# Optimization experiments

Measured on AMD Instinct MI355X. Metric: run time of the kernel, lower is better.

The kernel has to match this reference:

```python
import jax, jax.numpy as jnp
from jax import lax
import numpy as np

B = 512
IN_CAPS, OUT_CAPS, IN_DIM, OUT_DIM, ITERS = 32 * 6 * 6, 10, 8, 16, 3
EPS = 1e-8


def setup_inputs() -> dict:
    key = jax.random.key(0)
    ks = jax.random.split(key, 12)
    inp = {
        "x": jax.random.normal(ks[0], (B, 1, 28, 28), dtype=jnp.float32),
        "conv1_w": jax.random.normal(ks[1], (256, 1, 9, 9), dtype=jnp.float32) * 0.05,
        "conv1_b": jnp.zeros((256,), dtype=jnp.float32),
        "conv2_w": jax.random.normal(ks[2], (256, 256, 9, 9), dtype=jnp.float32) * 0.02,
        "conv2_b": jnp.zeros((256,), dtype=jnp.float32),
        "W": jax.random.normal(ks[3], (IN_CAPS, OUT_CAPS, IN_DIM, OUT_DIM), dtype=jnp.float32) * 0.1,
        "d1_w": jax.random.normal(ks[4], (OUT_DIM * OUT_CAPS, 512), dtype=jnp.float32) * 0.05,
        "d1_b": jnp.zeros((512,), dtype=jnp.float32),
        "d2_w": jax.random.normal(ks[5], (512, 1024), dtype=jnp.float32) * 0.05,
        "d2_b": jnp.zeros((1024,), dtype=jnp.float32),
        "d3_w": jax.random.normal(ks[6], (1024, 28 * 28), dtype=jnp.float32) * 0.05,
        "d3_b": jnp.zeros((28 * 28,), dtype=jnp.float32),
    }
    return inp


def _squash(s):
    # s2/(1+s2) * s/sqrt(s2+eps), norm over last dim
    s2 = jnp.sum(s * s, axis=-1, keepdims=True)
    return s2 / (1.0 + s2) * (s / jnp.sqrt(s2 + EPS))


def _conv(x, w, b, stride):
    y = lax.conv_general_dilated(x, w, (stride, stride), "VALID",
                                 dimension_numbers=("NCHW", "OIHW", "NCHW"))
    return y + b[None, :, None, None]


def reference(x, conv1_w, conv1_b, conv2_w, conv2_b, W,
              d1_w, d1_b, d2_w, d2_b, d3_w, d3_b):
    h = jax.nn.relu(_conv(x, conv1_w, conv1_b, 1))          # [B,256,20,20]
    h = _conv(h, conv2_w, conv2_b, 2)                       # [B,256,6,6]
    u = h.reshape(h.shape[0], 8, IN_CAPS).transpose(0, 2, 1)  # [B,1152,8]
    u = _squash(u)

    # dynamic routing
    u_hat = jnp.einsum("ijnm,bin->bijm", W, u)              # [B,1152,10,16]
    b_log = jnp.zeros((u.shape[0], IN_CAPS, OUT_CAPS), dtype=u.dtype)
    v = None
    for _ in range(ITERS):
        c = jax.nn.softmax(b_log, axis=1)                   # over in_capsules (as original)
        s = jnp.einsum("bij,bijm->bjm", c, u_hat)           # [B,10,16]
        v = _squash(s)
        b_log = b_log + jnp.einsum("bjm,bijm->bij", v, u_hat)
    caps = v                                                # [B,10,16]

    pred = jnp.argmax(jnp.sum(caps * caps, axis=-1), axis=-1)  # [B]
    mask = jax.lax.stop_gradient(jax.nn.one_hot(pred, OUT_CAPS, dtype=caps.dtype))
    dec_in = (caps * mask[:, :, None]).reshape(caps.shape[0], -1)  # [B,160]
    r = jax.nn.relu(dec_in @ d1_w + d1_b)
    r = jax.nn.relu(r @ d2_w + d2_b)
    r = jax.nn.sigmoid(r @ d3_w + d3_b)
    recon = r.reshape(-1, 1, 28, 28)
    return caps, recon, pred
```

## Files before the change

kernel.cpp:

```cpp
#include <hip/hip_runtime.h>

#define CAPS_EPS 1e-8f

typedef __attribute__((ext_vector_type(8))) short short8;
typedef __attribute__((ext_vector_type(4))) float f32x4;

__device__ inline ushort bf16_rn(float f) {
    uint u = __float_as_uint(f);
    u += 0x7fff + ((u >> 16) & 1);
    return (ushort)(u >> 16);
}
__device__ inline float bf16_f(ushort h) { return __uint_as_float((uint)h << 16); }

__device__ __forceinline__ void gld16(const void* g, void* l) {
    __builtin_amdgcn_global_load_lds(
        (const __attribute__((address_space(1))) unsigned int*)g,
        (__attribute__((address_space(3))) unsigned int*)l, 16, 0, 0);
}


__global__ __launch_bounds__(256) void k_pre(const float* __restrict__ w2,
                                             ushort* __restrict__ wBhi,
                                             ushort* __restrict__ wBlo,
                                             const float* __restrict__ x,
                                             ushort* __restrict__ xhi,
                                             ushort* __restrict__ xlo,
                                             const float* __restrict__ w1,
                                             ushort* __restrict__ w1phi,
                                             ushort* __restrict__ w1plo) {
    int bx = blockIdx.x, tid = threadIdx.x;
    if (bx < 256) {
        __shared__ float ld[81 * 65];
        int n = bx;
        const float* src = w2 + (size_t)n * 20736;
        for (int cc = 0; cc < 4; ++cc) {
            for (int i = tid; i < 5184; i += 256) {
                int c_loc = i / 81, t = i - c_loc * 81;
                ld[t * 65 + c_loc] = src[cc * 5184 + i];
            }
            __syncthreads();
            for (int i = tid; i < 5184; i += 256) {
                int t = i >> 6, c_loc = i & 63;
                float f = ld[t * 65 + c_loc];
                ushort hi = bf16_rn(f);
                ushort lo = bf16_rn(f - bf16_f(hi));
                size_t o = (size_t)n * 20736 + t * 256 + cc * 64 + c_loc;
                wBhi[o] = hi;
                wBlo[o] = lo;
            }
            __syncthreads();
        }
    } else if (bx < 256 + 1569) {
        int idx = (bx - 256) * 256 + tid;
        if (idx < 401408) {
            float f = x[idx];
            ushort hi = bf16_rn(f);
            ushort lo = bf16_rn(f - bf16_f(hi));
            xhi[idx] = hi;
            xlo[idx] = lo;
        } else if (idx < 401472) {
            xhi[idx] = 0;
            xlo[idx] = 0;
        }
    } else {
        int idx = (bx - 1825) * 256 + tid;
        int c = idx / 160;
        int kk160 = idx - c * 160;
        int kstep = kk160 >> 5, kk = kk160 & 31;
        int ky = kstep * 2 + (kk >> 4), kx = kk & 15;
        float f = (ky < 9 && kx < 9) ? w1[c * 81 + ky * 9 + kx] : 0.f;
        ushort hi = bf16_rn(f);
        ushort lo = bf16_rn(f - bf16_f(hi));
        w1phi[idx] = hi;
        w1plo[idx] = lo;
    }
}

__global__ __launch_bounds__(256) void k_conv1m(const ushort* __restrict__ xhi,
                                                const ushort* __restrict__ xlo,
                                                const ushort* __restrict__ w1phi,
                                                const ushort* __restrict__ w1plo,
                                                const float* __restrict__ b1,
                                                ushort* __restrict__ h1hi,
                                                ushort* __restrict__ h1lo) {
    int tid = threadIdx.x;
    int wv = tid >> 6, lane = tid & 63;
    int lrow = lane & 15, quad = lane >> 4;
    int m0 = blockIdx.x * 128 + wv * 32;
    int c0 = blockIdx.y * 64;

    int am[2];
#pragma unroll
    for (int t = 0; t < 2; ++t) {
        int m = m0 + t * 16 + lrow;
        int b = m / 400, r = m - b * 400;
        int y = r / 20, xx = r - y * 20;
        am[t] = b * 784 + y * 28 + xx;
    }

    f32x4 acc[2][4];
#pragma unroll
    for (int t = 0; t < 2; ++t)
#pragma unroll
        for (int tn = 0; tn < 4; ++tn) acc[t][tn] = (f32x4){0.f, 0.f, 0.f, 0.f};

    for (int kstep = 0; kstep < 5; ++kstep) {
        int arow = (kstep * 2 + (quad >> 1)) * 28 + (quad & 1) * 8;
        int boff = kstep * 32 + quad * 8;
        short8 bh[4], bl2[4];
#pragma unroll
        for (int tn = 0; tn < 4; ++tn) {
            int br = (c0 + tn * 16 + lrow) * 160 + boff;
            bh[tn] = *reinterpret_cast<const short8*>(w1phi + br);
            bl2[tn] = *reinterpret_cast<const short8*>(w1plo + br);
        }
#pragma unroll
        for (int t = 0; t < 2; ++t) {
            short8 ah = *reinterpret_cast<const short8*>(xhi + am[t] + arow);
            short8 al = *reinterpret_cast<const short8*>(xlo + am[t] + arow);
#pragma unroll
            for (int tn = 0; tn < 4; ++tn) {
                acc[t][tn] = __builtin_amdgcn_mfma_f32_16x16x32_bf16(ah, bh[tn], acc[t][tn], 0, 0, 0);
                acc[t][tn] = __builtin_amdgcn_mfma_f32_16x16x32_bf16(ah, bl2[tn], acc[t][tn], 0, 0, 0);
                acc[t][tn] = __builtin_amdgcn_mfma_f32_16x16x32_bf16(al, bh[tn], acc[t][tn], 0, 0, 0);
            }
        }
    }

#pragma unroll
    for (int t = 0; t < 2; ++t)
#pragma unroll
        for (int r = 0; r < 4; ++r) {
            int m = m0 + t * 16 + quad * 4 + r;
#pragma unroll
            for (int tn = 0; tn < 4; ++tn) {
                int c = c0 + tn * 16 + lrow;
                float v = acc[t][tn][r] + b1[c];
                v = fmaxf(v, 0.f);
                ushort hi = bf16_rn(v);
                ushort lo = bf16_rn(v - bf16_f(hi));
                h1hi[(size_t)m * 256 + c] = hi;
                h1lo[(size_t)m * 256 + c] = lo;
            }
        }
}

__global__ __launch_bounds__(256) void k_h2init(const float* __restrict__ b2,
                                                float* __restrict__ h2) {
    h2[(size_t)blockIdx.x * 256 + threadIdx.x] = b2[threadIdx.x];
}

__global__ __launch_bounds__(256) void k_zero4(float* __restrict__ p) {
    reinterpret_cast<float4*>(p)[(size_t)blockIdx.x * 256 + threadIdx.x] = make_float4(0, 0, 0, 0);
}

__global__ __launch_bounds__(256, 2) void k_conv2m(const ushort* __restrict__ h1hi,
                                                   const ushort* __restrict__ h1lo,
                                                   const ushort* __restrict__ wBhi,
                                                   const ushort* __restrict__ wBlo,
                                                   float* __restrict__ h2) {
    __shared__ ushort Ahi[128 * 32];
    __shared__ ushort Alo[128 * 32];
    __shared__ ushort Bhi[256 * 32];
    __shared__ ushort Blo[256 * 32];
    int tid = threadIdx.x;
    int m0 = blockIdx.x * 128;
    int kbase = blockIdx.y * 2592;

    int wv = tid >> 6, lane = tid & 63;
    int cq = (lane & 3) * 8;

    int ra = wv * 32 + (lane >> 2);
    int mA0 = m0 + ra, mA1 = mA0 + 16;
    int mb0 = mA0 / 36, mp0 = mA0 - mb0 * 36;
    int mb1 = mA1 / 36, mp1 = mA1 - mb1 * 36;
    size_t a0 = ((size_t)mb0 * 400 + (mp0 / 6) * 40 + (mp0 % 6) * 2) * 256 + cq;
    size_t a1 = ((size_t)mb1 * 400 + (mp1 / 6) * 40 + (mp1 % 6) * 2) * 256 + cq;
    int ldsA = wv * 1024;

    int rb = wv * 64 + (lane >> 2);
    size_t bB = (size_t)rb * 20736 + cq;
    int ldsB = wv * 2048;

    int mhalf = (wv >> 1) * 64, nhalf = (wv & 1) * 128;
    int lrow = lane & 15, quad = lane >> 4;

    f32x4 acc[4][8];
#pragma unroll
    for (int a = 0; a < 4; ++a)
#pragma unroll
        for (int bq = 0; bq < 8; ++bq) acc[a][bq] = (f32x4){0.f, 0.f, 0.f, 0.f};

    for (int ks = 0; ks < 81; ++ks) {
        int k = kbase + ks * 32;
        int t = k >> 8, cc = k & 255;
        int ky = t / 9, kx = t - ky * 9;
        size_t koffA = (size_t)(ky * 5120 + kx * 256 + cc);

        __syncthreads();
        gld16(h1hi + a0 + koffA, &Ahi[ldsA]);
        gld16(h1hi + a1 + koffA, &Ahi[ldsA + 512]);
        gld16(h1lo + a0 + koffA, &Alo[ldsA]);
        gld16(h1lo + a1 + koffA, &Alo[ldsA + 512]);
#pragma unroll
        for (int q = 0; q < 4; ++q) {
            size_t bo = bB + (size_t)q * 331776 + k;
            gld16(wBhi + bo, &Bhi[ldsB + q * 512]);
            gld16(wBlo + bo, &Blo[ldsB + q * 512]);
        }
        __syncthreads();

        short8 ah[4], al[4];
#pragma unroll
        for (int tm = 0; tm < 4; ++tm) {
            int off = (mhalf + tm * 16 + lrow) * 32 + quad * 8;
            ah[tm] = *reinterpret_cast<short8*>(&Ahi[off]);
            al[tm] = *reinterpret_cast<short8*>(&Alo[off]);
        }
#pragma unroll
        for (int tn = 0; tn < 8; ++tn) {
            int off = (nhalf + tn * 16 + lrow) * 32 + quad * 8;
            short8 bh = *reinterpret_cast<short8*>(&Bhi[off]);
            short8 bl2 = *reinterpret_cast<short8*>(&Blo[off]);
#pragma unroll
            for (int tm = 0; tm < 4; ++tm) {
                acc[tm][tn] = __builtin_amdgcn_mfma_f32_16x16x32_bf16(ah[tm], bh, acc[tm][tn], 0, 0, 0);
                acc[tm][tn] = __builtin_amdgcn_mfma_f32_16x16x32_bf16(ah[tm], bl2, acc[tm][tn], 0, 0, 0);
                acc[tm][tn] = __builtin_amdgcn_mfma_f32_16x16x32_bf16(al[tm], bh, acc[tm][tn], 0, 0, 0);
            }
        }
    }

#pragma unroll
    for (int tm = 0; tm < 4; ++tm) {
        int mrow = m0 + mhalf + tm * 16 + quad * 4;
#pragma unroll
        for (int tn = 0; tn < 8; ++tn) {
            int ncol = nhalf + tn * 16 + lrow;
#pragma unroll
            for (int r = 0; r < 4; ++r)
                atomicAdd(&h2[(size_t)(mrow + r) * 256 + ncol], acc[tm][tn][r]);
        }
    }
}

__global__ __launch_bounds__(256) void k_squashT2(const float* __restrict__ h2,
                                                  float* __restrict__ uT) {
    __shared__ float ld[32][257];
    __shared__ float scl[32][33];
    int s = blockIdx.x;
    int b0 = blockIdx.y * 32;
    int t = threadIdx.x;
    for (int bb = 0; bb < 32; ++bb)
        ld[bb][t] = h2[((size_t)(b0 + bb) * 36 + s) * 256 + t];
    __syncthreads();
    int b = t & 31, gb = (t >> 5) * 4;
#pragma unroll
    for (int q = 0; q < 4; ++q) {
        int g = gb + q;
        float s2 = 0.f;
#pragma unroll
        for (int n = 0; n < 8; ++n) {
            float vv = ld[b][g + n * 32];
            s2 = fmaf(vv, vv, s2);
        }
        scl[b][g] = s2 / ((1.f + s2) * sqrtf(s2 + CAPS_EPS));
    }
    __syncthreads();
    int hf = t >> 5;
    for (int gg = 0; gg < 32; ++gg) {
        int idx = hf * 32 + gg;
        int g = idx >> 3, n = idx & 7;
        uT[(((size_t)g * 36 + s) * 8 + n) * 512 + b0 + b] = ld[b][g + n * 32] * scl[b][g];
    }
}

__global__ __launch_bounds__(256) void k_s(const float* __restrict__ Wc,
                                           const float* __restrict__ uT,
                                           const float* __restrict__ bl,
                                           const float* __restrict__ Z,
                                           float* __restrict__ sT,
                                           int first) {
    __shared__ float lw[8 * 1280];
    int tid = threadIdx.x;
    int i0 = blockIdx.x * 8;
    int b = blockIdx.y * 128 + (tid & 127);
    int mh = tid >> 7;
    const float* wg = Wc + (size_t)i0 * 1280;
#pragma unroll
    for (int r = 0; r < 10; ++r) {
        int q4 = (r * 256 + tid) * 4;
        *reinterpret_cast<float4*>(&lw[q4]) = *reinterpret_cast<const float4*>(wg + q4);
    }
    __syncthreads();
    float rzs[10];
    if (!first) {
#pragma unroll
        for (int j = 0; j < 10; ++j) rzs[j] = 1.0f / Z[j * 512 + b];
    }
    float acc[80];
#pragma unroll
    for (int q = 0; q < 80; ++q) acc[q] = 0.f;
    for (int di = 0; di < 8; ++di) {
        int i = i0 + di;
        float ur[8];
#pragma unroll
        for (int n = 0; n < 8; ++n) ur[n] = uT[((size_t)i * 8 + n) * 512 + b];
#pragma unroll
        for (int j = 0; j < 10; ++j) {
            float c;
            if (first) c = (1.0f / 1152.0f);
            else c = expf(bl[((size_t)i * 10 + j) * 512 + b]) * rzs[j];
            const float* wp = &lw[(di * 10 + j) * 128 + mh * 8];
            float4 s0 = {0.f, 0.f, 0.f, 0.f}, s1 = {0.f, 0.f, 0.f, 0.f};
#pragma unroll
            for (int n = 0; n < 8; ++n) {
                const float4* wq = reinterpret_cast<const float4*>(wp + n * 16);
                float4 wa = wq[0], wb = wq[1];
                float un = ur[n];
                s0.x = fmaf(un, wa.x, s0.x); s0.y = fmaf(un, wa.y, s0.y);
                s0.z = fmaf(un, wa.z, s0.z); s0.w = fmaf(un, wa.w, s0.w);
                s1.x = fmaf(un, wb.x, s1.x); s1.y = fmaf(un, wb.y, s1.y);
                s1.z = fmaf(un, wb.z, s1.z); s1.w = fmaf(un, wb.w, s1.w);
            }
            acc[j * 8 + 0] = fmaf(c, s0.x, acc[j * 8 + 0]);
            acc[j * 8 + 1] = fmaf(c, s0.y, acc[j * 8 + 1]);
            acc[j * 8 + 2] = fmaf(c, s0.z, acc[j * 8 + 2]);
            acc[j * 8 + 3] = fmaf(c, s0.w, acc[j * 8 + 3]);
            acc[j * 8 + 4] = fmaf(c, s1.x, acc[j * 8 + 4]);
            acc[j * 8 + 5] = fmaf(c, s1.y, acc[j * 8 + 5]);
            acc[j * 8 + 6] = fmaf(c, s1.z, acc[j * 8 + 6]);
            acc[j * 8 + 7] = fmaf(c, s1.w, acc[j * 8 + 7]);
        }
    }
#pragma unroll
    for (int j = 0; j < 10; ++j)
#pragma unroll
        for (int mm = 0; mm < 8; ++mm)
            atomicAdd(&sT[(j * 16 + mh * 8 + mm) * 512 + b], acc[j * 8 + mm]);
}

__global__ __launch_bounds__(256) void k_v(const float* __restrict__ sT,
                                           float* __restrict__ v,
                                           float* __restrict__ vT,
                                           float* __restrict__ sTz,
                                           float* __restrict__ Z) {
    int idx = blockIdx.x * 256 + threadIdx.x;
    int j = idx >> 9;
    int b = idx & 511;
    float sv[16];
    float s2 = 0.f;
#pragma unroll
    for (int m = 0; m < 16; ++m) {
        sv[m] = sT[(j * 16 + m) * 512 + b];
        s2 = fmaf(sv[m], sv[m], s2);
    }
    float scale = s2 / ((1.f + s2) * sqrtf(s2 + CAPS_EPS));
#pragma unroll
    for (int m = 0; m < 16; ++m) {
        float val = sv[m] * scale;
        v[(size_t)b * 160 + j * 16 + m] = val;
        vT[(j * 16 + m) * 512 + b] = val;
        sTz[(j * 16 + m) * 512 + b] = 0.f;
    }
    Z[idx] = 0.f;
}

__global__ __launch_bounds__(256) void k_bupd(const float* __restrict__ Wc,
                                              const float* __restrict__ uT,
                                              const float* __restrict__ vT,
                                              float* __restrict__ bl,
                                              float* __restrict__ Z) {
    __shared__ float lw[8 * 1280];
    int tid = threadIdx.x;
    int i0 = blockIdx.x * 8;
    int b = blockIdx.y * 128 + (tid & 127);
    int ih = tid >> 7;
    const float* wg = Wc + (size_t)i0 * 1280;
#pragma unroll
    for (int r = 0; r < 10; ++r) {
        int q4 = (r * 256 + tid) * 4;
        *reinterpret_cast<float4*>(&lw[q4]) = *reinterpret_cast<const float4*>(wg + q4);
    }
    __syncthreads();
    float ur[4][8];
#pragma unroll
    for (int ii = 0; ii < 4; ++ii) {
        int i = i0 + ih * 4 + ii;
#pragma unroll
        for (int n = 0; n < 8; ++n) ur[ii][n] = uT[((size_t)i * 8 + n) * 512 + b];
    }
    for (int j = 0; j < 10; ++j) {
        float vj[16];
#pragma unroll
        for (int m = 0; m < 16; ++m) vj[m] = vT[(j * 16 + m) * 512 + b];
        float zp = 0.f;
#pragma unroll
        for (int ii = 0; ii < 4; ++ii) {
            int di = ih * 4 + ii;
            const float* wp = &lw[(di * 10 + j) * 128];
            float t = 0.f;
#pragma unroll
            for (int n = 0; n < 8; ++n) {
                const float4* wq = reinterpret_cast<const float4*>(wp + n * 16);
                float4 w0 = wq[0], w1 = wq[1], w2 = wq[2], w3 = wq[3];
                float wvv = w0.x * vj[0];
                wvv = fmaf(w0.y, vj[1], wvv);  wvv = fmaf(w0.z, vj[2], wvv);
                wvv = fmaf(w0.w, vj[3], wvv);  wvv = fmaf(w1.x, vj[4], wvv);
                wvv = fmaf(w1.y, vj[5], wvv);  wvv = fmaf(w1.z, vj[6], wvv);
                wvv = fmaf(w1.w, vj[7], wvv);  wvv = fmaf(w2.x, vj[8], wvv);
                wvv = fmaf(w2.y, vj[9], wvv);  wvv = fmaf(w2.z, vj[10], wvv);
                wvv = fmaf(w2.w, vj[11], wvv); wvv = fmaf(w3.x, vj[12], wvv);
                wvv = fmaf(w3.y, vj[13], wvv); wvv = fmaf(w3.z, vj[14], wvv);
                wvv = fmaf(w3.w, vj[15], wvv);
                t = fmaf(ur[ii][n], wvv, t);
            }
            size_t idx = ((size_t)(i0 + di) * 10 + j) * 512 + b;
            float nb = bl[idx] + t;
            bl[idx] = nb;
            zp += expf(nb);
        }
        atomicAdd(&Z[j * 512 + b], zp);
    }
}

__global__ __launch_bounds__(256) void k_pred(const float* __restrict__ v,
                                              float* __restrict__ out,
                                              float* __restrict__ dec,
                                              int pred_off) {
    int b = blockIdx.x, t = threadIdx.x;
    __shared__ float sq[160];
    __shared__ float nrm[10];
    __shared__ int ip;
    float val = 0.f;
    if (t < 160) {
        val = v[(size_t)b * 160 + t];
        out[(size_t)b * 160 + t] = val;
        sq[t] = val * val;
    }
    __syncthreads();
    if (t < 10) {
        float s = 0.f;
#pragma unroll
        for (int k = 0; k < 16; ++k) s += sq[t * 16 + k];
        nrm[t] = s;
    }
    __syncthreads();
    if (t == 0) {
        float best = nrm[0];
        int bi = 0;
        for (int j = 1; j < 10; ++j)
            if (nrm[j] > best) { best = nrm[j]; bi = j; }
        ip = bi;
        out[(size_t)pred_off + b] = (float)bi;
    }
    __syncthreads();
    if (t < 160) dec[(size_t)b * 160 + t] = ((t >> 4) == ip) ? val : 0.f;
}

template <int ACT>
__global__ __launch_bounds__(256) void k_gemm(const float* __restrict__ A,
                                              const float* __restrict__ B,
                                              const float* __restrict__ bias,
                                              float* __restrict__ C,
                                              int M, int K, int N) {
    __shared__ float As[16 * 64];
    __shared__ float Bs[16 * 64];
    int tid = threadIdx.x;
    int m0 = blockIdx.y * 64, n0 = blockIdx.x * 64;
    int arow = tid >> 2, akq = (tid & 3) * 4;
    int brow = tid >> 4, bcol = (tid & 15) * 4;
    int ty = tid >> 4, tx = tid & 15;
    float acc[4][4];
#pragma unroll
    for (int r = 0; r < 4; ++r)
#pragma unroll
        for (int q = 0; q < 4; ++q) acc[r][q] = 0.f;
    for (int k0 = 0; k0 < K; k0 += 16) {
        float4 av = *reinterpret_cast<const float4*>(A + (size_t)(m0 + arow) * K + k0 + akq);
        float4 bv = make_float4(0, 0, 0, 0);
        if (n0 + bcol < N)
            bv = *reinterpret_cast<const float4*>(B + (size_t)(k0 + brow) * N + n0 + bcol);
        __syncthreads();
        As[(akq + 0) * 64 + arow] = av.x;
        As[(akq + 1) * 64 + arow] = av.y;
        As[(akq + 2) * 64 + arow] = av.z;
        As[(akq + 3) * 64 + arow] = av.w;
        *reinterpret_cast<float4*>(&Bs[brow * 64 + bcol]) = bv;
        __syncthreads();
#pragma unroll
        for (int kk = 0; kk < 16; ++kk) {
            float4 a4 = *reinterpret_cast<float4*>(&As[kk * 64 + ty * 4]);
            float4 b4 = *reinterpret_cast<float4*>(&Bs[kk * 64 + tx * 4]);
            float ar[4] = {a4.x, a4.y, a4.z, a4.w};
            float br[4] = {b4.x, b4.y, b4.z, b4.w};
#pragma unroll
            for (int r = 0; r < 4; ++r)
#pragma unroll
                for (int q = 0; q < 4; ++q)
                    acc[r][q] = fmaf(ar[r], br[q], acc[r][q]);
        }
    }
#pragma unroll
    for (int r = 0; r < 4; ++r) {
        int mm = m0 + ty * 4 + r;
#pragma unroll
        for (int q = 0; q < 4; ++q) {
            int nn = n0 + tx * 4 + q;
            if (nn < N) {
                float val = acc[r][q] + bias[nn];
                if (ACT == 0) val = fmaxf(val, 0.f);
                else val = 1.f / (1.f + expf(-val));
                C[(size_t)mm * N + nn] = val;
            }
        }
    }
}

extern "C" void kernel_launch(void* const* d_in, const int* in_sizes, int n_in,
                              void* d_out, int out_size, void* d_ws, size_t ws_size,
                              hipStream_t stream) {
    const float* x   = (const float*)d_in[0];
    const float* w1  = (const float*)d_in[1];
    const float* b1  = (const float*)d_in[2];
    const float* w2  = (const float*)d_in[3];
    const float* b2  = (const float*)d_in[4];
    const float* Wc  = (const float*)d_in[5];
    const float* d1w = (const float*)d_in[6];
    const float* d1b = (const float*)d_in[7];
    const float* d2w = (const float*)d_in[8];
    const float* d2b = (const float*)d_in[9];
    const float* d3w = (const float*)d_in[10];
    const float* d3b = (const float*)d_in[11];
    float* out = (float*)d_out;

    ushort* wBhi = (ushort*)d_ws;
    ushort* wBlo = wBhi + 5308416;
    ushort* h1hi = (ushort*)((char*)d_ws + 21233664);
    ushort* h1lo = h1hi + 52428800;
    char*   h2b  = (char*)d_ws + 230948864;
    float*  h2   = (float*)h2b;
    ushort* xhi   = (ushort*)h2b;
    ushort* xlo   = xhi + 401472;
    ushort* w1phi = xlo + 401472;
    ushort* w1plo = w1phi + 40960;

    float* post = (float*)((char*)d_ws + 21233664);
    float* uT  = post + 4718592;
    float* bl  = post + 9437184;
    float* sT  = post + 15335424;
    float* Z   = post + 15417344;
    float* v   = post + 15422464;
    float* vT  = post + 15504384;
    float* dec = post + 15586304;
    float* r1  = post + 15668224;
    float* r2  = post + 15930368;

    int pred_off = out_size - 512;

    k_pre<<<1985, 256, 0, stream>>>(w2, wBhi, wBlo, x, xhi, xlo, w1, w1phi, w1plo);
    k_conv1m<<<dim3(1600, 4), 256, 0, stream>>>(xhi, xlo, w1phi, w1plo, b1, h1hi, h1lo);
    k_h2init<<<18432, 256, 0, stream>>>(b2, h2);
    k_conv2m<<<dim3(144, 8), 256, 0, stream>>>(h1hi, h1lo, wBhi, wBlo, h2);
    k_zero4<<<5845, 256, 0, stream>>>(bl);
    k_squashT2<<<dim3(36, 16), 256, 0, stream>>>(h2, uT);

    for (int it = 0; it < 3; ++it) {
        k_s<<<dim3(144, 4), 256, 0, stream>>>(Wc, uT, bl, Z, sT, it == 0 ? 1 : 0);
        k_v<<<20, 256, 0, stream>>>(sT, v, vT, sT, Z);
        if (it < 2) k_bupd<<<dim3(144, 4), 256, 0, stream>>>(Wc, uT, vT, bl, Z);
    }

    k_pred<<<512, 256, 0, stream>>>(v, out, dec, pred_off);
    k_gemm<0><<<dim3(8, 8), 256, 0, stream>>>(dec, d1w, d1b, r1, 512, 160, 512);
    k_gemm<0><<<dim3(16, 8), 256, 0, stream>>>(r1, d2w, d2b, r2, 512, 512, 1024);
    k_gemm<1><<<dim3(13, 8), 256, 0, stream>>>(r2, d3w, d3b, out + 81920, 512, 1024, 784);
}
```

Measured before the change: 1.373 ms.

## Move decoder GEMMs to split-bf16 MFMA and fuse post-conv setup kernels

Replaces the three fp32 SIMT decoder GEMMs with MFMA GEMMs that use hi/lo bf16 splitting (three products) to keep near-fp32 accuracy. The decoder weights are transposed and split by a new merged k_post kernel, which also does the squash-transpose and the zeroing of the routing logits, so two launches go away. The h2 bias init is vectorised to float4, and the conv2 grid axes are swapped so consecutive blocks share the same M tile, which may change L2 reuse and atomic contention. The weight transposes are redone on every call and add extra memory traffic.

```diff
diff --git a/kernel.cpp b/kernel.cpp
--- a/kernel.cpp
+++ b/kernel.cpp
@@ -145,13 +145,11 @@
         }
 }
 
-__global__ __launch_bounds__(256) void k_h2init(const float* __restrict__ b2,
-                                                float* __restrict__ h2) {
-    h2[(size_t)blockIdx.x * 256 + threadIdx.x] = b2[threadIdx.x];
-}
-
-__global__ __launch_bounds__(256) void k_zero4(float* __restrict__ p) {
-    reinterpret_cast<float4*>(p)[(size_t)blockIdx.x * 256 + threadIdx.x] = make_float4(0, 0, 0, 0);
+__global__ __launch_bounds__(256) void k_h2init4(const float* __restrict__ b2,
+                                                 float* __restrict__ h2) {
+    size_t idx = (size_t)blockIdx.x * 256 + threadIdx.x;
+    const float4* b24 = reinterpret_cast<const float4*>(b2);
+    reinterpret_cast<float4*>(h2)[idx] = b24[idx & 63];
 }
 
 __global__ __launch_bounds__(256, 2) void k_conv2m(const ushort* __restrict__ h1hi,
@@ -164,8 +162,8 @@
     __shared__ ushort Bhi[256 * 32];
     __shared__ ushort Blo[256 * 32];
     int tid = threadIdx.x;
-    int m0 = blockIdx.x * 128;
-    int kbase = blockIdx.y * 2592;
+    int m0 = blockIdx.y * 128;
+    int kbase = blockIdx.x * 2592;
 
     int wv = tid >> 6, lane = tid & 63;
     int cq = (lane & 3) * 8;
@@ -244,34 +242,80 @@
     }
 }
 
-__global__ __launch_bounds__(256) void k_squashT2(const float* __restrict__ h2,
-                                                  float* __restrict__ uT) {
-    __shared__ float ld[32][257];
-    __shared__ float scl[32][33];
-    int s = blockIdx.x;
-    int b0 = blockIdx.y * 32;
-    int t = threadIdx.x;
-    for (int bb = 0; bb < 32; ++bb)
-        ld[bb][t] = h2[((size_t)(b0 + bb) * 36 + s) * 256 + t];
+__device__ __forceinline__ void wtrans(const float* __restrict__ src,
+                                       ushort* __restrict__ dh,
+                                       ushort* __restrict__ dl,
+                                       float* ld, int kt, int nt, int K, int N,
+                                       int tid) {
+    for (int i = tid; i < 4096; i += 256) {
+        int kk = i >> 6, nn = i & 63;
+        int k = kt * 64 + kk, n = nt * 64 + nn;
+        float f = (k < K && n < N) ? src[(size_t)k * N + n] : 0.f;
+        ld[kk * 65 + nn] = f;
+    }
     __syncthreads();
-    int b = t & 31, gb = (t >> 5) * 4;
-#pragma unroll
-    for (int q = 0; q < 4; ++q) {
-        int g = gb + q;
-        float s2 = 0.f;
-#pragma unroll
-        for (int n = 0; n < 8; ++n) {
-            float vv = ld[b][g + n * 32];
-            s2 = fmaf(vv, vv, s2);
-        }
-        scl[b][g] = s2 / ((1.f + s2) * sqrtf(s2 + CAPS_EPS));
-    }
-    __syncthreads();
-    int hf = t >> 5;
-    for (int gg = 0; gg < 32; ++gg) {
-        int idx = hf * 32 + gg;
-        int g = idx >> 3, n = idx & 7;
-        uT[(((size_t)g * 36 + s) * 8 + n) * 512 + b0 + b] = ld[b][g + n * 32] * scl[b][g];
+    for (int i = tid; i < 4096; i += 256) {
+        int nn = i >> 6, kk = i & 63;
+        int k = kt * 64 + kk, n = nt * 64 + nn;
+        if (k < K) {
+            float f = ld[kk * 65 + nn];
+            ushort hi = bf16_rn(f);
+            ushort lo = bf16_rn(f - bf16_f(hi));
+            dh[(size_t)n * K + k] = hi;
+            dl[(size_t)n * K + k] = lo;
+        }
+    }
+}
+
+__global__ __launch_bounds__(256) void k_post(const float* __restrict__ h2,
+                                              float* __restrict__ uT,
+                                              float* __restrict__ zr,
+                                              const float* __restrict__ d1w,
+                                              const float* __restrict__ d2w,
+                                              const float* __restrict__ d3w,
+                                              ushort* __restrict__ d1wThi, ushort* __restrict__ d1wTlo,
+                                              ushort* __restrict__ d2wThi, ushort* __restrict__ d2wTlo,
+                                              ushort* __restrict__ d3wThi, ushort* __restrict__ d3wTlo) {
+    __shared__ float smem[8224 + 1056];
+    int bx = blockIdx.x, t = threadIdx.x;
+    if (bx < 576) {
+        float (*ld)[257] = (float (*)[257])smem;
+        float (*scl)[33] = (float (*)[33])(smem + 8224);
+        int s = bx % 36;
+        int b0 = (bx / 36) * 32;
+        for (int bb = 0; bb < 32; ++bb)
+            ld[bb][t] = h2[((size_t)(b0 + bb) * 36 + s) * 256 + t];
+        __syncthreads();
+        int b = t & 31, gb = (t >> 5) * 4;
+#pragma unroll
+        for (int q = 0; q < 4; ++q) {
+            int g = gb + q;
+            float s2 = 0.f;
+#pragma unroll
+            for (int n = 0; n < 8; ++n) {
+                float vv = ld[b][g + n * 32];
+                s2 = fmaf(vv, vv, s2);
+            }
+            scl[b][g] = s2 / ((1.f + s2) * sqrtf(s2 + CAPS_EPS));
+        }
+        __syncthreads();
+        int hf = t >> 5;
+        for (int gg = 0; gg < 32; ++gg) {
+            int idx = hf * 32 + gg;
+            int g = idx >> 3, n = idx & 7;
+            uT[(((size_t)g * 36 + s) * 8 + n) * 512 + b0 + b] = ld[b][g + n * 32] * scl[b][g];
+        }
+    } else if (bx < 6421) {
+        reinterpret_cast<float4*>(zr)[(size_t)(bx - 576) * 256 + t] = make_float4(0, 0, 0, 0);
+    } else if (bx < 6445) {
+        int local = bx - 6421;
+        wtrans(d1w, d1wThi, d1wTlo, smem, local / 8, local % 8, 160, 512, t);
+    } else if (bx < 6573) {
+        int local = bx - 6445;
+        wtrans(d2w, d2wThi, d2wTlo, smem, local / 16, local % 16, 512, 1024, t);
+    } else {
+        int local = bx - 6573;
+        wtrans(d3w, d3wThi, d3wTlo, smem, local / 14, local % 14, 1024, 784, t);
     }
 }
 
@@ -426,7 +470,8 @@
 
 __global__ __launch_bounds__(256) void k_pred(const float* __restrict__ v,
                                               float* __restrict__ out,
-                                              float* __restrict__ dec,
+                                              ushort* __restrict__ dechi,
+                                              ushort* __restrict__ declo,
                                               int pred_off) {
     int b = blockIdx.x, t = threadIdx.x;
     __shared__ float sq[160];
@@ -455,66 +500,83 @@
         out[(size_t)pred_off + b] = (float)bi;
     }
     __syncthreads();
-    if (t < 160) dec[(size_t)b * 160 + t] = ((t >> 4) == ip) ? val : 0.f;
-}
-
-template <int ACT>
-__global__ __launch_bounds__(256) void k_gemm(const float* __restrict__ A,
-                                              const float* __restrict__ B,
-                                              const float* __restrict__ bias,
-                                              float* __restrict__ C,
-                                              int M, int K, int N) {
-    __shared__ float As[16 * 64];
-    __shared__ float Bs[16 * 64];
+    if (t < 160) {
+        float d = ((t >> 4) == ip) ? val : 0.f;
+        ushort hi = bf16_rn(d);
+        ushort lo = bf16_rn(d - bf16_f(hi));
+        dechi[(size_t)b * 160 + t] = hi;
+        declo[(size_t)b * 160 + t] = lo;
+    }
+}
+
+template <int ACT, int SPLIT_OUT>
+__global__ __launch_bounds__(256) void k_gemmm(const ushort* __restrict__ Ahi,
+                                               const ushort* __restrict__ Alo,
+                                               const ushort* __restrict__ Bhi,
+                                               const ushort* __restrict__ Blo,
+                                               const float* __restrict__ bias,
+                                               ushort* __restrict__ Chi,
+                                               ushort* __restrict__ Clo,
+                                               float* __restrict__ Cf,
+                                               int K, int Ng) {
     int tid = threadIdx.x;
-    int m0 = blockIdx.y * 64, n0 = blockIdx.x * 64;
-    int arow = tid >> 2, akq = (tid & 3) * 4;
-    int brow = tid >> 4, bcol = (tid & 15) * 4;
-    int ty = tid >> 4, tx = tid & 15;
-    float acc[4][4];
-#pragma unroll
-    for (int r = 0; r < 4; ++r)
-#pragma unroll
-        for (int q = 0; q < 4; ++q) acc[r][q] = 0.f;
-    for (int k0 = 0; k0 < K; k0 += 16) {
-        float4 av = *reinterpret_cast<const float4*>(A + (size_t)(m0 + arow) * K + k0 + akq);
-        float4 bv = make_float4(0, 0, 0, 0);
-        if (n0 + bcol < N)
-            bv = *reinterpret_cast<const float4*>(B + (size_t)(k0 + brow) * N + n0 + bcol);
-        __syncthreads();
-        As[(akq + 0) * 64 + arow] = av.x;
-        As[(akq + 1) * 64 + arow] = av.y;
-        As[(akq + 2) * 64 + arow] = av.z;
-        As[(akq + 3) * 64 + arow] = av.w;
-        *reinterpret_cast<float4*>(&Bs[brow * 64 + bcol]) = bv;
-        __syncthreads();
-#pragma unroll
-        for (int kk = 0; kk < 16; ++kk) {
-            float4 a4 = *reinterpret_cast<float4*>(&As[kk * 64 + ty * 4]);
-            float4 b4 = *reinterpret_cast<float4*>(&Bs[kk * 64 + tx * 4]);
-            float ar[4] = {a4.x, a4.y, a4.z, a4.w};
-            float br[4] = {b4.x, b4.y, b4.z, b4.w};
-#pragma unroll
-            for (int r = 0; r < 4; ++r)
-#pragma unroll
-                for (int q = 0; q < 4; ++q)
-                    acc[r][q] = fmaf(ar[r], br[q], acc[r][q]);
-        }
-    }
-#pragma unroll
-    for (int r = 0; r < 4; ++r) {
-        int mm = m0 + ty * 4 + r;
-#pragma unroll
-        for (int q = 0; q < 4; ++q) {
-            int nn = n0 + tx * 4 + q;
-            if (nn < N) {
-                float val = acc[r][q] + bias[nn];
-                if (ACT == 0) val = fmaxf(val, 0.f);
-                else val = 1.f / (1.f + expf(-val));
-                C[(size_t)mm * N + nn] = val;
-            }
-        }
-    }
+    int wv = tid >> 6, lane = tid & 63;
+    int lrow = lane & 15, quad = lane >> 4;
+    int m0 = blockIdx.x * 64 + (wv >> 1) * 32;
+    int n0 = blockIdx.y * 128 + (wv & 1) * 64;
+
+    f32x4 acc[2][4];
+#pragma unroll
+    for (int t = 0; t < 2; ++t)
+#pragma unroll
+        for (int tn = 0; tn < 4; ++tn) acc[t][tn] = (f32x4){0.f, 0.f, 0.f, 0.f};
+
+    for (int ks = 0; ks < K; ks += 32) {
+        int boff = ks + quad * 8;
+        short8 bh[4], bl2[4];
+#pragma unroll
+        for (int tn = 0; tn < 4; ++tn) {
+            size_t br = (size_t)(n0 + tn * 16 + lrow) * K + boff;
+            bh[tn] = *reinterpret_cast<const short8*>(Bhi + br);
+            bl2[tn] = *reinterpret_cast<const short8*>(Blo + br);
+        }
+#pragma unroll
+        for (int t = 0; t < 2; ++t) {
+            size_t ar = (size_t)(m0 + t * 16 + lrow) * K + boff;
+            short8 ah = *reinterpret_cast<const short8*>(Ahi + ar);
+            short8 al = *reinterpret_cast<const short8*>(Alo + ar);
+#pragma unroll
+            for (int tn = 0; tn < 4; ++tn) {
+                acc[t][tn] = __builtin_amdgcn_mfma_f32_16x16x32_bf16(ah, bh[tn], acc[t][tn], 0, 0, 0);
+                acc[t][tn] = __builtin_amdgcn_mfma_f32_16x16x32_bf16(ah, bl2[tn], acc[t][tn], 0, 0, 0);
+                acc[t][tn] = __builtin_amdgcn_mfma_f32_16x16x32_bf16(al, bh[tn], acc[t][tn], 0, 0, 0);
+            }
+        }
+    }
+
+#pragma unroll
+    for (int t = 0; t < 2; ++t)
+#pragma unroll
+        for (int r = 0; r < 4; ++r) {
+            int m = m0 + t * 16 + quad * 4 + r;
+#pragma unroll
+            for (int tn = 0; tn < 4; ++tn) {
+                int n = n0 + tn * 16 + lrow;
+                if (n < Ng) {
+                    float val = acc[t][tn][r] + bias[n];
+                    if (ACT == 0) val = fmaxf(val, 0.f);
+                    else val = 1.f / (1.f + expf(-val));
+                    if (SPLIT_OUT) {
+                        ushort hi = bf16_rn(val);
+                        ushort lo = bf16_rn(val - bf16_f(hi));
+                        Chi[(size_t)m * Ng + n] = hi;
+                        Clo[(size_t)m * Ng + n] = lo;
+                    } else {
+                        Cf[(size_t)m * Ng + n] = val;
+                    }
+                }
+            }
+        }
 }
 
 extern "C" void kernel_launch(void* const* d_in, const int* in_sizes, int n_in,
@@ -552,18 +614,28 @@
     float* Z   = post + 15417344;
     float* v   = post + 15422464;
     float* vT  = post + 15504384;
-    float* dec = post + 15586304;
-    float* r1  = post + 15668224;
-    float* r2  = post + 15930368;
+    ushort* ub = (ushort*)(post + 15586304);
+    ushort* dechi   = ub;
+    ushort* declo   = ub + 81920;
+    ushort* r1hi    = ub + 163840;
+    ushort* r1lo    = ub + 425984;
+    ushort* r2hi    = ub + 688128;
+    ushort* r2lo    = ub + 1212416;
+    ushort* d1wThi  = ub + 1736704;
+    ushort* d1wTlo  = ub + 1818624;
+    ushort* d2wThi  = ub + 1900544;
+    ushort* d2wTlo  = ub + 2424832;
+    ushort* d3wThi  = ub + 2949120;
+    ushort* d3wTlo  = ub + 3866624;
 
     int pred_off = out_size - 512;
 
     k_pre<<<1985, 256, 0, stream>>>(w2, wBhi, wBlo, x, xhi, xlo, w1, w1phi, w1plo);
     k_conv1m<<<dim3(1600, 4), 256, 0, stream>>>(xhi, xlo, w1phi, w1plo, b1, h1hi, h1lo);
-    k_h2init<<<18432, 256, 0, stream>>>(b2, h2);
-    k_conv2m<<<dim3(144, 8), 256, 0, stream>>>(h1hi, h1lo, wBhi, wBlo, h2);
-    k_zero4<<<5845, 256, 0, stream>>>(bl);
-    k_squashT2<<<dim3(36, 16), 256, 0, stream>>>(h2, uT);
+    k_h2init4<<<4608, 256, 0, stream>>>(b2, h2);
+    k_conv2m<<<dim3(8, 144), 256, 0, stream>>>(h1hi, h1lo, wBhi, wBlo, h2);
+    k_post<<<6797, 256, 0, stream>>>(h2, uT, bl, d1w, d2w, d3w,
+                                     d1wThi, d1wTlo, d2wThi, d2wTlo, d3wThi, d3wTlo);
 
     for (int it = 0; it < 3; ++it) {
         k_s<<<dim3(144, 4), 256, 0, stream>>>(Wc, uT, bl, Z, sT, it == 0 ? 1 : 0);
@@ -571,8 +643,11 @@
         if (it < 2) k_bupd<<<dim3(144, 4), 256, 0, stream>>>(Wc, uT, vT, bl, Z);
     }
 
-    k_pred<<<512, 256, 0, stream>>>(v, out, dec, pred_off);
-    k_gemm<0><<<dim3(8, 8), 256, 0, stream>>>(dec, d1w, d1b, r1, 512, 160, 512);
-    k_gemm<0><<<dim3(16, 8), 256, 0, stream>>>(r1, d2w, d2b, r2, 512, 512, 1024);
-    k_gemm<1><<<dim3(13, 8), 256, 0, stream>>>(r2, d3w, d3b, out + 81920, 512, 1024, 784);
-}
+    k_pred<<<512, 256, 0, stream>>>(v, out, dechi, declo, pred_off);
+    k_gemmm<0, 1><<<dim3(8, 4), 256, 0, stream>>>(dechi, declo, d1wThi, d1wTlo, d1b,
+                                                  r1hi, r1lo, nullptr, 160, 512);
+    k_gemmm<0, 1><<<dim3(8, 8), 256, 0, stream>>>(r1hi, r1lo, d2wThi, d2wTlo, d2b,
+                                                  r2hi, r2lo, nullptr, 512, 1024);
+    k_gemmm<1, 0><<<dim3(8, 7), 256, 0, stream>>>(r2hi, r2lo, d3wThi, d3wTlo, d3b,
+                                                  nullptr, nullptr, out + 81920, 1024, 784);
+}
```

Measured after the change: 1.372 ms. About the same (-0.1%).
